# Kernel optimization log

Measured on AMD Instinct MI355X. Metric: run time of the kernel, lower is better.

Reference implementation:

```python
import jax, jax.numpy as jnp
import numpy as np

E = 1024  # embedding_dim
QD = 1024  # query_dim (also key dim)
VD = 1024  # value_dim
B, S = 4, 2048


def setup_inputs() -> dict:
    key = jax.random.key(0)
    k1, k2, k3, k4, k5, k6, k7, k8 = jax.random.split(key, 8)
    x = jax.random.normal(k1, (B, S, E), dtype=jnp.float32)
    mask = jax.random.randint(k2, (B, S, S), 0, 2, dtype=jnp.int32)
    s = 1.0 / np.sqrt(E)
    Wq = jax.random.uniform(k3, (E, QD), jnp.float32, -s, s)
    bq = jax.random.uniform(k4, (QD,), jnp.float32, -s, s)
    Wk = jax.random.uniform(k5, (E, QD), jnp.float32, -s, s)
    bk = jax.random.uniform(k6, (QD,), jnp.float32, -s, s)
    Wv = jax.random.uniform(k7, (E, VD), jnp.float32, -s, s)
    bv = jax.random.uniform(k8, (VD,), jnp.float32, -s, s)
    return {"x": x, "mask": mask, "Wq": Wq, "bq": bq, "Wk": Wk, "bk": bk, "Wv": Wv, "bv": bv}


def reference(x, mask, Wq, bq, Wk, bk, Wv, bv):
    # projections: [B,S,E] @ [E,D] -> [B,S,D]
    q = jnp.einsum('bse,ed->bsd', x, Wq) + bq
    k = jnp.einsum('bse,ed->bsd', x, Wk) + bk
    v = jnp.einsum('bse,ed->bsd', x, Wv) + bv
    # scores scaled by query_dim (NOT sqrt(query_dim)), per original code
    weights = jnp.einsum('bqd,bkd->bqk', q, k) / QD
    weights = jnp.where(mask == 0, -jnp.inf, weights)
    weights = jax.nn.softmax(weights, axis=-1)
    out = jnp.einsum('bqk,bkd->bqd', weights, v)
    return out
```

## Files before the change

kernel.cpp:

```cpp
#include <hip/hip_runtime.h>
#include <hip/hip_bf16.h>


typedef __bf16 bf16x8 __attribute__((ext_vector_type(8)));
typedef __bf16 bf16x4 __attribute__((ext_vector_type(4)));
typedef float f32x4 __attribute__((ext_vector_type(4)));

#define BM 128
#define BN 128
#define BK 64

__device__ inline void glds16(const __bf16* g, __bf16* l) {
    __builtin_amdgcn_global_load_lds(
        (const __attribute__((address_space(1))) unsigned int*)g,
        (__attribute__((address_space(3))) unsigned int*)l,
        16, 0, 0);
}

template <int EPI>
__global__ __launch_bounds__(512, 2) void gemm256(
    const __bf16* __restrict__ A, const __bf16* __restrict__ B,
    __bf16* __restrict__ C0, __bf16* __restrict__ C1,
    const float* __restrict__ bias0, const float* __restrict__ bias1,
    int K, int ldc, float scale, long sA, long sB, long sC)
{
    A += (long)blockIdx.z * sA;
    B += (long)blockIdx.z * sB;

    __shared__ __align__(16) char sm[131072];

    const int t = threadIdx.x;
    const int w = t >> 6, l = t & 63;
    const int wm = w >> 2, wn = w & 3;
    const int row0 = blockIdx.x * 256, col0 = blockIdx.y * 256;
    const int srow = l >> 3;
    const int skel = (((l & 7) ^ srow) & 7) * 8;
    const int lm = l & 15, g16 = l >> 4, sx = lm & 7;

    const __bf16* Ap = A + (size_t)row0 * K;
    const __bf16* Bp = B + (size_t)col0 * K;

    f32x4 acc[8][4];
#pragma unroll
    for (int i = 0; i < 8; i++)
#pragma unroll
        for (int j = 0; j < 4; j++) acc[i][j] = (f32x4){0.f, 0.f, 0.f, 0.f};

    auto stageHalf = [&](int mat, int h, int buf, int kt) {
        const __bf16* G = mat ? Bp : Ap;
        char* base = sm + (buf << 16) + mat * 32768 + h * 16384;
#pragma unroll
        for (int i = 0; i < 2; i++) {
            const int c = w * 2 + i;
            glds16(G + (size_t)(h * 128 + c * 8 + srow) * K + kt + skel,
                   (__bf16*)(base + c * 1024));
        }
    };

    bf16x8 a03[4][2], a47[4][2], b01[2][2], b23[2][2];

    auto rdA = [&](bf16x8 (&d)[4][2], int buf, int half) {
        const char* Ab = sm + (buf << 16);
#pragma unroll
        for (int mt = 0; mt < 4; mt++) {
            const int r = wm * 128 + half * 64 + mt * 16 + lm;
#pragma unroll
            for (int ks = 0; ks < 2; ks++)
                d[mt][ks] = *(const bf16x8*)(Ab + r * 128 + ((((ks << 2) | g16) ^ sx) << 4));
        }
    };
    auto rdB = [&](bf16x8 (&d)[2][2], int buf, int half) {
        const char* Bb = sm + (buf << 16) + 32768;
#pragma unroll
        for (int nt = 0; nt < 2; nt++) {
            const int r = wn * 64 + half * 32 + nt * 16 + lm;
#pragma unroll
            for (int ks = 0; ks < 2; ks++)
                d[nt][ks] = *(const bf16x8*)(Bb + r * 128 + ((((ks << 2) | g16) ^ sx) << 4));
        }
    };
    auto mf8 = [&](bf16x8 (&Af)[4][2], bf16x8 (&Bf)[2][2], int mo, int no) {
#pragma unroll
        for (int ks = 0; ks < 2; ks++)
#pragma unroll
            for (int mt = 0; mt < 4; mt++)
#pragma unroll
                for (int nt = 0; nt < 2; nt++)
                    acc[mo + mt][no + nt] = __builtin_amdgcn_mfma_f32_16x16x32_bf16(
                        Af[mt][ks], Bf[nt][ks], acc[mo + mt][no + nt], 0, 0, 0);
    };

#define SB    __builtin_amdgcn_sched_barrier(0)
#define BAR   __builtin_amdgcn_s_barrier()
#define VM4   asm volatile("s_waitcnt vmcnt(4)")

    stageHalf(0, 0, 0, 0); stageHalf(0, 1, 0, 0);
    stageHalf(1, 0, 0, 0); stageHalf(1, 1, 0, 0);
    stageHalf(0, 0, 1, 64); stageHalf(0, 1, 1, 64);
    SB; VM4; BAR; SB;

    const int nkt = K >> 6;
    for (int tt = 0; tt < nkt; tt += 2) {
#pragma unroll
        for (int sub = 0; sub < 2; sub++) {
            const int tcur = tt + sub;
            const int buf = sub;
            const int ktn1 = (tcur + 1) << 6;
            const int ktn2 = (tcur + 2) << 6;
            rdA(a03, buf, 0); rdB(b01, buf, 0);
            stageHalf(1, 0, buf ^ 1, ktn1);
            SB; BAR; SB;
            __builtin_amdgcn_s_setprio(1); mf8(a03, b01, 0, 0); __builtin_amdgcn_s_setprio(0);
            SB; BAR; SB;
            rdA(a47, buf, 1); rdB(b23, buf, 1);
            stageHalf(1, 1, buf ^ 1, ktn1);
            SB; BAR; SB;
            __builtin_amdgcn_s_setprio(1); mf8(a47, b01, 4, 0); __builtin_amdgcn_s_setprio(0);
            SB; BAR; SB;
            stageHalf(0, 0, buf, ktn2);
            SB; BAR; SB;
            __builtin_amdgcn_s_setprio(1); mf8(a03, b23, 0, 2); __builtin_amdgcn_s_setprio(0);
            SB; BAR; SB;
            stageHalf(0, 1, buf, ktn2);
            SB; BAR; SB;
            __builtin_amdgcn_s_setprio(1); mf8(a47, b23, 4, 2); __builtin_amdgcn_s_setprio(0);
            SB; VM4; BAR; SB;
        }
    }
#undef SB
#undef BAR
#undef VM4

    float* smC = (float*)sm;
    const int rl = g16 * 4;
    float breg[4];
    __bf16* Cout;
    int cbase;
    if (EPI == 0) {
        const bool isQ = (col0 < 1024);
        const float* bias = isQ ? bias0 : bias1;
        cbase = col0 & 1023;
        Cout = isQ ? C0 : C1;
#pragma unroll
        for (int nt = 0; nt < 4; nt++) breg[nt] = bias[cbase + wn * 64 + nt * 16 + lm];
    } else {
        Cout = C0 + (long)blockIdx.z * sC;
        cbase = col0;
    }

#pragma unroll
    for (int mt = 0; mt < 8; mt++) {
#pragma unroll
        for (int nt = 0; nt < 4; nt++)
#pragma unroll
            for (int i = 0; i < 4; i++) {
                const int lr = wm * 16 + rl + i;
                const int c = wn * 64 + nt * 16 + lm;
                float v = acc[mt][nt][i];
                if (EPI == 0) v += breg[nt];
                if (EPI == 4) v *= scale;
                smC[lr * 260 + c] = v;
            }
        __syncthreads();
#pragma unroll
        for (int r = 0; r < 4; r++) {
            const int rr = r * 8 + w;
            const float4 v4 = *(const float4*)&smC[rr * 260 + l * 4];
            bf16x4 o = {(__bf16)v4.x, (__bf16)v4.y, (__bf16)v4.z, (__bf16)v4.w};
            const int gr = row0 + (rr >> 4) * 128 + mt * 16 + (rr & 15);
            *(bf16x4*)&Cout[(size_t)gr * ldc + cbase + l * 4] = o;
        }
        __syncthreads();
    }
}

template <int EPI>
__global__ __launch_bounds__(256) void gemm_bt(
    const __bf16* __restrict__ A, const __bf16* __restrict__ B,
    float* __restrict__ Cf, __bf16* __restrict__ Cb,
    const float* __restrict__ bias,
    int M, int N, int K, float scale,
    long sA, long sB, long sC)
{
    A += (long)blockIdx.z * sA;
    B += (long)blockIdx.z * sB;
    if (EPI == 3) Cf += (long)blockIdx.z * sC;
    if (EPI == 4) Cb += (long)blockIdx.z * sC;

    __shared__ __align__(16) char smraw[65536];
    float* smC = (float*)smraw;

    const int t = threadIdx.x;
    const int w = t >> 6;
    const int l = t & 63;
    const int row0 = blockIdx.x * BM;
    const int col0 = blockIdx.y * BN;
    const int wm = (w >> 1) * 64;
    const int wn = (w & 1) * 64;

    const int srow = l >> 3;
    const int skel = (((l & 7) ^ srow) & 7) * 8;

    const int lm = l & 15;
    const int g16 = l >> 4;
    const int sx = lm & 7;

    f32x4 acc[4][4];
#pragma unroll
    for (int i = 0; i < 4; i++)
#pragma unroll
        for (int j = 0; j < 4; j++) acc[i][j] = (f32x4){0.f, 0.f, 0.f, 0.f};

    auto stage = [&](int buf, int kt) {
        __bf16* sA = (__bf16*)(smraw + buf * 32768);
        __bf16* sB = sA + BM * BK;
#pragma unroll
        for (int i = 0; i < 4; i++) {
            const int chunk = i * 4 + w;
            const int r = chunk * 8 + srow;
            glds16(A + (size_t)(row0 + r) * K + kt + skel, &sA[chunk * 512]);
            glds16(B + (size_t)(col0 + r) * K + kt + skel, &sB[chunk * 512]);
        }
    };

    stage(0, 0);
    int cur = 0;
    for (int kt = 0; kt < K; kt += BK) {
        __syncthreads();
        if (kt + BK < K) stage(cur ^ 1, kt + BK);

        const __bf16* sA = (const __bf16*)(smraw + cur * 32768);
        const __bf16* sB = sA + BM * BK;
#pragma unroll
        for (int ks = 0; ks < 2; ks++) {
            bf16x8 af[4], bg[4];
            const int p = ((ks * 4 + g16) ^ sx) * 8;
#pragma unroll
            for (int mt = 0; mt < 4; mt++)
                af[mt] = *(const bf16x8*)&sA[(wm + mt * 16 + lm) * BK + p];
#pragma unroll
            for (int nt = 0; nt < 4; nt++)
                bg[nt] = *(const bf16x8*)&sB[(wn + nt * 16 + lm) * BK + p];
#pragma unroll
            for (int mt = 0; mt < 4; mt++)
#pragma unroll
                for (int nt = 0; nt < 4; nt++)
                    acc[mt][nt] = __builtin_amdgcn_mfma_f32_16x16x32_bf16(
                        af[mt], bg[nt], acc[mt][nt], 0, 0, 0);
        }
        cur ^= 1;
    }
    __syncthreads();

    const int rl = (l >> 4) * 4;
    float breg[4];
    if (EPI <= 1) {
#pragma unroll
        for (int nt = 0; nt < 4; nt++) breg[nt] = bias[col0 + wn + nt * 16 + lm];
    }
#pragma unroll
    for (int mt = 0; mt < 4; mt++) {
#pragma unroll
        for (int nt = 0; nt < 4; nt++)
#pragma unroll
            for (int i = 0; i < 4; i++) {
                const int lr = (w >> 1) * 16 + rl + i;
                const int c  = wn + nt * 16 + lm;
                float v = acc[mt][nt][i];
                if (EPI <= 1) v += breg[nt];
                if (EPI == 4) v *= scale;
                smC[lr * 132 + c] = v;
            }
        __syncthreads();

        if (EPI == 1) {
#pragma unroll
            for (int k = 0; k < 4; k++) {
                const int d  = (t >> 3) + 32 * k;
                const int sc = (t & 7) * 4;
                const int gr = row0 + mt * 16 + (sc & 15) + (sc >> 4) * 64;
                bf16x4 o;
#pragma unroll
                for (int j = 0; j < 4; j++) o[j] = (__bf16)smC[(sc + j) * 132 + d];
                *(bf16x4*)&Cb[(size_t)(gr >> 11) * ((size_t)N * 2048)
                              + (size_t)(col0 + d) * 2048 + (gr & 2047)] = o;
            }
        } else {
#pragma unroll
            for (int k = 0; k < 4; k++) {
                const int lr = (t >> 5) + 8 * k;
                const int c4 = (t & 31) * 4;
                const int gr = row0 + mt * 16 + (lr & 15) + (lr >> 4) * 64;
                const float4 v = *(const float4*)&smC[lr * 132 + c4];
                if (EPI == 0 || EPI == 4) {
                    bf16x4 o = {(__bf16)v.x, (__bf16)v.y, (__bf16)v.z, (__bf16)v.w};
                    *(bf16x4*)&Cb[(size_t)gr * N + col0 + c4] = o;
                } else {
                    *(float4*)&Cf[(size_t)gr * N + col0 + c4] = v;
                }
            }
        }
        __syncthreads();
    }
}

__global__ __launch_bounds__(256) void cast_x(const float* __restrict__ X, __bf16* __restrict__ Y) {
    const size_t i = (size_t)blockIdx.x * 256 + threadIdx.x;
    const float4* X4 = (const float4*)X;
    const float4 a = X4[i * 2], b = X4[i * 2 + 1];
    bf16x8 o = {(__bf16)a.x, (__bf16)a.y, (__bf16)a.z, (__bf16)a.w,
                (__bf16)b.x, (__bf16)b.y, (__bf16)b.z, (__bf16)b.w};
    ((bf16x8*)Y)[i] = o;
}

__global__ void cast_wt(const float* __restrict__ Wq, const float* __restrict__ Wk,
                        const float* __restrict__ Wv, __bf16* __restrict__ Wt) {
    const float* W = blockIdx.z == 0 ? Wq : (blockIdx.z == 1 ? Wk : Wv);
    __bf16* O = Wt + (size_t)blockIdx.z * 1024 * 1024;
    __shared__ float tile[32][33];
    const int tx = threadIdx.x, ty = threadIdx.y;
    const int d0 = blockIdx.x * 32, e0 = blockIdx.y * 32;
#pragma unroll
    for (int j = 0; j < 32; j += 8)
        tile[ty + j][tx] = W[(size_t)(e0 + ty + j) * 1024 + d0 + tx];
    __syncthreads();
#pragma unroll
    for (int j = 0; j < 32; j += 8)
        O[(size_t)(d0 + ty + j) * 1024 + e0 + tx] = (__bf16)tile[tx][ty + j];
}

__global__ __launch_bounds__(256) void softmax_rows(const __bf16* __restrict__ S,
                                                    const int* __restrict__ mask,
                                                    __bf16* __restrict__ P) {
    const size_t row = blockIdx.x;
    const int t = threadIdx.x;
    const int w = t >> 6, l = t & 63;
    const bf16x8 s8 = ((const bf16x8*)(S + row * 2048))[t];
    const int4 mk0 = ((const int4*)(mask + row * 2048))[t * 2];
    const int4 mk1 = ((const int4*)(mask + row * 2048))[t * 2 + 1];
    float v[8];
    v[0] = mk0.x ? (float)s8[0] : -1e30f;
    v[1] = mk0.y ? (float)s8[1] : -1e30f;
    v[2] = mk0.z ? (float)s8[2] : -1e30f;
    v[3] = mk0.w ? (float)s8[3] : -1e30f;
    v[4] = mk1.x ? (float)s8[4] : -1e30f;
    v[5] = mk1.y ? (float)s8[5] : -1e30f;
    v[6] = mk1.z ? (float)s8[6] : -1e30f;
    v[7] = mk1.w ? (float)s8[7] : -1e30f;
    float m = v[0];
#pragma unroll
    for (int i = 1; i < 8; i++) m = fmaxf(m, v[i]);
#pragma unroll
    for (int off = 32; off; off >>= 1) m = fmaxf(m, __shfl_xor(m, off, 64));
    __shared__ float rm[4], rs[4];
    if (l == 0) rm[w] = m;
    __syncthreads();
    m = fmaxf(fmaxf(rm[0], rm[1]), fmaxf(rm[2], rm[3]));
    float e[8], sum = 0.f;
#pragma unroll
    for (int i = 0; i < 8; i++) { e[i] = __expf(v[i] - m); sum += e[i]; }
#pragma unroll
    for (int off = 32; off; off >>= 1) sum += __shfl_xor(sum, off, 64);
    if (l == 0) rs[w] = sum;
    __syncthreads();
    const float inv = 1.f / (rs[0] + rs[1] + rs[2] + rs[3]);
    bf16x8 o;
#pragma unroll
    for (int i = 0; i < 8; i++) o[i] = (__bf16)(e[i] * inv);
    ((bf16x8*)(P + row * 2048))[t] = o;
}

extern "C" void kernel_launch(void* const* d_in, const int* in_sizes, int n_in,
                              void* d_out, int out_size, void* d_ws, size_t ws_size,
                              hipStream_t stream) {
    const float* x  = (const float*)d_in[0];
    const int* mask = (const int*)d_in[1];
    const float* Wq = (const float*)d_in[2];
    const float* bq = (const float*)d_in[3];
    const float* Wk = (const float*)d_in[4];
    const float* bk = (const float*)d_in[5];
    const float* Wv = (const float*)d_in[6];
    const float* bv = (const float*)d_in[7];
    float* out = (float*)d_out;

    char* ws = (char*)d_ws;
    __bf16* xb = (__bf16*)(ws);
    __bf16* Wt = (__bf16*)(ws + (16ull << 20));
    __bf16* Qb = (__bf16*)(ws + (22ull << 20));
    __bf16* Kb = (__bf16*)(ws + (38ull << 20));
    __bf16* Vt = (__bf16*)(ws + (54ull << 20));
    __bf16* Sf = (__bf16*)(ws + (70ull << 20));
    __bf16* Pb = (__bf16*)(ws + (22ull << 20));

    cast_x<<<4096, 256, 0, stream>>>(x, xb);
    cast_wt<<<dim3(32, 32, 3), dim3(32, 8), 0, stream>>>(Wq, Wk, Wv, Wt);

    gemm256<0><<<dim3(32, 8, 1), 512, 0, stream>>>(xb, Wt, Qb, Kb, bq, bk,
                                                   1024, 1024, 1.f, 0, 0, 0);
    gemm_bt<1><<<dim3(64, 8, 1), 256, 0, stream>>>(xb, Wt + (2u << 20), nullptr, Vt, bv,
                                                   8192, 1024, 1024, 1.f, 0, 0, 0);

    gemm256<4><<<dim3(8, 8, 4), 512, 0, stream>>>(Qb, Kb, Sf, nullptr, nullptr, nullptr,
                                                  1024, 2048, 1.0f / 1024.0f,
                                                  2048L * 1024, 2048L * 1024,
                                                  2048L * 2048);

    softmax_rows<<<8192, 256, 0, stream>>>(Sf, mask, Pb);

    gemm_bt<3><<<dim3(16, 8, 4), 256, 0, stream>>>(Pb, Vt, out, nullptr, nullptr,
                                                   2048, 1024, 2048, 1.f,
                                                   2048L * 2048, 1024L * 2048,
                                                   2048L * 1024);
}
```

Before: 306.9 us.

## Use inline ds_read with explicit lgkmcnt waits and merge cast kernels

Replaces the compiler-generated LDS fragment loads in the 256-tile GEMM with inline-asm ds_read_b128 plus an explicit lgkmcnt(0) wait after each barrier, so the schedule controls LDS latency instead of the compiler. It also adds a vmcnt(0) drain and barrier before the epilogue, which reuses shared memory. The x cast and the weight transpose-cast are merged into one launch to cut launch overhead. Unused EPI 0/4 paths are removed from gemm_bt.

```diff
diff --git a/kernel.cpp b/kernel.cpp
--- a/kernel.cpp
+++ b/kernel.cpp
@@ -15,6 +15,14 @@
         (const __attribute__((address_space(1))) unsigned int*)g,
         (__attribute__((address_space(3))) unsigned int*)l,
         16, 0, 0);
+}
+
+typedef const __attribute__((address_space(3))) char* lds_cptr;
+
+__device__ inline bf16x8 dsr16(lds_cptr p) {
+    f32x4 r;
+    asm volatile("ds_read_b128 %0, %1" : "=v"(r) : "v"(p));
+    return __builtin_bit_cast(bf16x8, r);
 }
 
 template <int EPI>
@@ -28,6 +36,7 @@
     B += (long)blockIdx.z * sB;
 
     __shared__ __align__(16) char sm[131072];
+    lds_cptr sml = (lds_cptr)sm;
 
     const int t = threadIdx.x;
     const int w = t >> 6, l = t & 63;
@@ -60,23 +69,23 @@
     bf16x8 a03[4][2], a47[4][2], b01[2][2], b23[2][2];
 
     auto rdA = [&](bf16x8 (&d)[4][2], int buf, int half) {
-        const char* Ab = sm + (buf << 16);
+        lds_cptr Ab = sml + (buf << 16);
 #pragma unroll
         for (int mt = 0; mt < 4; mt++) {
             const int r = wm * 128 + half * 64 + mt * 16 + lm;
 #pragma unroll
             for (int ks = 0; ks < 2; ks++)
-                d[mt][ks] = *(const bf16x8*)(Ab + r * 128 + ((((ks << 2) | g16) ^ sx) << 4));
+                d[mt][ks] = dsr16(Ab + r * 128 + ((((ks << 2) | g16) ^ sx) << 4));
         }
     };
     auto rdB = [&](bf16x8 (&d)[2][2], int buf, int half) {
-        const char* Bb = sm + (buf << 16) + 32768;
+        lds_cptr Bb = sml + (buf << 16) + 32768;
 #pragma unroll
         for (int nt = 0; nt < 2; nt++) {
             const int r = wn * 64 + half * 32 + nt * 16 + lm;
 #pragma unroll
             for (int ks = 0; ks < 2; ks++)
-                d[nt][ks] = *(const bf16x8*)(Bb + r * 128 + ((((ks << 2) | g16) ^ sx) << 4));
+                d[nt][ks] = dsr16(Bb + r * 128 + ((((ks << 2) | g16) ^ sx) << 4));
         }
     };
     auto mf8 = [&](bf16x8 (&Af)[4][2], bf16x8 (&Bf)[2][2], int mo, int no) {
@@ -92,6 +101,7 @@
 
 #define SB    __builtin_amdgcn_sched_barrier(0)
 #define BAR   __builtin_amdgcn_s_barrier()
+#define LGKM0 asm volatile("s_waitcnt lgkmcnt(0)")
 #define VM4   asm volatile("s_waitcnt vmcnt(4)")
 
     stageHalf(0, 0, 0, 0); stageHalf(0, 1, 0, 0);
@@ -109,12 +119,12 @@
             const int ktn2 = (tcur + 2) << 6;
             rdA(a03, buf, 0); rdB(b01, buf, 0);
             stageHalf(1, 0, buf ^ 1, ktn1);
-            SB; BAR; SB;
+            SB; BAR; LGKM0; SB;
             __builtin_amdgcn_s_setprio(1); mf8(a03, b01, 0, 0); __builtin_amdgcn_s_setprio(0);
             SB; BAR; SB;
             rdA(a47, buf, 1); rdB(b23, buf, 1);
             stageHalf(1, 1, buf ^ 1, ktn1);
-            SB; BAR; SB;
+            SB; BAR; LGKM0; SB;
             __builtin_amdgcn_s_setprio(1); mf8(a47, b01, 4, 0); __builtin_amdgcn_s_setprio(0);
             SB; BAR; SB;
             stageHalf(0, 0, buf, ktn2);
@@ -127,8 +137,11 @@
             SB; VM4; BAR; SB;
         }
     }
+    asm volatile("s_waitcnt vmcnt(0)");
+    SB; BAR; SB;
 #undef SB
 #undef BAR
+#undef LGKM0
 #undef VM4
 
     float* smC = (float*)sm;
@@ -185,7 +198,6 @@
     A += (long)blockIdx.z * sA;
     B += (long)blockIdx.z * sB;
     if (EPI == 3) Cf += (long)blockIdx.z * sC;
-    if (EPI == 4) Cb += (long)blockIdx.z * sC;
 
     __shared__ __align__(16) char smraw[65536];
     float* smC = (float*)smraw;
@@ -254,7 +266,7 @@
 
     const int rl = (l >> 4) * 4;
     float breg[4];
-    if (EPI <= 1) {
+    if (EPI == 1) {
 #pragma unroll
         for (int nt = 0; nt < 4; nt++) breg[nt] = bias[col0 + wn + nt * 16 + lm];
     }
@@ -267,8 +279,7 @@
                 const int lr = (w >> 1) * 16 + rl + i;
                 const int c  = wn + nt * 16 + lm;
                 float v = acc[mt][nt][i];
-                if (EPI <= 1) v += breg[nt];
-                if (EPI == 4) v *= scale;
+                if (EPI == 1) v += breg[nt];
                 smC[lr * 132 + c] = v;
             }
         __syncthreads();
@@ -292,41 +303,43 @@
                 const int c4 = (t & 31) * 4;
                 const int gr = row0 + mt * 16 + (lr & 15) + (lr >> 4) * 64;
                 const float4 v = *(const float4*)&smC[lr * 132 + c4];
-                if (EPI == 0 || EPI == 4) {
-                    bf16x4 o = {(__bf16)v.x, (__bf16)v.y, (__bf16)v.z, (__bf16)v.w};
-                    *(bf16x4*)&Cb[(size_t)gr * N + col0 + c4] = o;
-                } else {
-                    *(float4*)&Cf[(size_t)gr * N + col0 + c4] = v;
-                }
+                *(float4*)&Cf[(size_t)gr * N + col0 + c4] = v;
             }
         }
         __syncthreads();
     }
 }
 
-__global__ __launch_bounds__(256) void cast_x(const float* __restrict__ X, __bf16* __restrict__ Y) {
-    const size_t i = (size_t)blockIdx.x * 256 + threadIdx.x;
-    const float4* X4 = (const float4*)X;
-    const float4 a = X4[i * 2], b = X4[i * 2 + 1];
-    bf16x8 o = {(__bf16)a.x, (__bf16)a.y, (__bf16)a.z, (__bf16)a.w,
-                (__bf16)b.x, (__bf16)b.y, (__bf16)b.z, (__bf16)b.w};
-    ((bf16x8*)Y)[i] = o;
-}
-
-__global__ void cast_wt(const float* __restrict__ Wq, const float* __restrict__ Wk,
-                        const float* __restrict__ Wv, __bf16* __restrict__ Wt) {
-    const float* W = blockIdx.z == 0 ? Wq : (blockIdx.z == 1 ? Wk : Wv);
-    __bf16* O = Wt + (size_t)blockIdx.z * 1024 * 1024;
+__global__ __launch_bounds__(256) void cast_all(
+    const float* __restrict__ X, __bf16* __restrict__ Y,
+    const float* __restrict__ Wq, const float* __restrict__ Wk,
+    const float* __restrict__ Wv, __bf16* __restrict__ Wt)
+{
     __shared__ float tile[32][33];
-    const int tx = threadIdx.x, ty = threadIdx.y;
-    const int d0 = blockIdx.x * 32, e0 = blockIdx.y * 32;
-#pragma unroll
-    for (int j = 0; j < 32; j += 8)
-        tile[ty + j][tx] = W[(size_t)(e0 + ty + j) * 1024 + d0 + tx];
-    __syncthreads();
-#pragma unroll
-    for (int j = 0; j < 32; j += 8)
-        O[(size_t)(d0 + ty + j) * 1024 + e0 + tx] = (__bf16)tile[tx][ty + j];
+    const int t = threadIdx.x;
+    if (blockIdx.x < 4096) {
+        const size_t i = (size_t)blockIdx.x * 256 + t;
+        const float4* X4 = (const float4*)X;
+        const float4 a = X4[i * 2], b = X4[i * 2 + 1];
+        bf16x8 o = {(__bf16)a.x, (__bf16)a.y, (__bf16)a.z, (__bf16)a.w,
+                    (__bf16)b.x, (__bf16)b.y, (__bf16)b.z, (__bf16)b.w};
+        ((bf16x8*)Y)[i] = o;
+    } else {
+        const int b = blockIdx.x - 4096;
+        const int z = b >> 10;
+        const int bb = b & 1023;
+        const float* W = z == 0 ? Wq : (z == 1 ? Wk : Wv);
+        __bf16* O = Wt + (size_t)z * 1024 * 1024;
+        const int tx = t & 31, ty = t >> 5;
+        const int d0 = (bb & 31) * 32, e0 = (bb >> 5) * 32;
+#pragma unroll
+        for (int j = 0; j < 32; j += 8)
+            tile[ty + j][tx] = W[(size_t)(e0 + ty + j) * 1024 + d0 + tx];
+        __syncthreads();
+#pragma unroll
+        for (int j = 0; j < 32; j += 8)
+            O[(size_t)(d0 + ty + j) * 1024 + e0 + tx] = (__bf16)tile[tx][ty + j];
+    }
 }
 
 __global__ __launch_bounds__(256) void softmax_rows(const __bf16* __restrict__ S,
@@ -392,11 +405,11 @@
     __bf16* Sf = (__bf16*)(ws + (70ull << 20));
     __bf16* Pb = (__bf16*)(ws + (22ull << 20));
 
-    cast_x<<<4096, 256, 0, stream>>>(x, xb);
-    cast_wt<<<dim3(32, 32, 3), dim3(32, 8), 0, stream>>>(Wq, Wk, Wv, Wt);
+    cast_all<<<7168, 256, 0, stream>>>(x, xb, Wq, Wk, Wv, Wt);
 
     gemm256<0><<<dim3(32, 8, 1), 512, 0, stream>>>(xb, Wt, Qb, Kb, bq, bk,
                                                    1024, 1024, 1.f, 0, 0, 0);
+
     gemm_bt<1><<<dim3(64, 8, 1), 256, 0, stream>>>(xb, Wt + (2u << 20), nullptr, Vt, bv,
                                                    8192, 1024, 1024, 1.f, 0, 0, 0);
 
```

Result: slower. 322.6 us (+5.1%).
